# Kernel tuning notes

Hardware: AMD Instinct MI355X
Metric: run time of the kernel (lower is better)

The kernel has to match this reference:

```python
import jax, jax.numpy as jnp
import numpy as np

B, N1, N2, E = 8, 32, 32, 256
H = 8                 # num_heads == args.vir_heads
KD = E // H           # key dim per head = 32
HD = E // H           # head dim (value_dim == embed_dim)
L = N1 * N2           # 1024 tokens
SCALING = KD ** -0.5
LN_EPS = 1e-5


def _rel_pos_2d():
    # RetNetRelPosDeform2D with zero offsets (vir_use_deformable=False)
    half = 1.0 / 10000.0 ** jnp.linspace(0.0, 1.0, KD // 2)
    angle = jnp.repeat(half, 2)                                   # (KD,) interleaved pairs
    decay = jnp.log(1.0 - 2.0 ** (-2.0 - 5.0 * jnp.arange(H, dtype=jnp.float32) / H))  # (H,)
    i1 = jnp.arange(N1, dtype=jnp.float32)
    i2 = jnp.arange(N2, dtype=jnp.float32)
    index_k = (i1[:, None] + i2[None, :]).reshape(L)              # (L,)
    sin_k = jnp.sin(index_k[:, None] * angle[None, :])            # (L, KD)
    cos_k = jnp.cos(index_k[:, None] * angle[None, :])
    # zero offsets => index_q == index_k, broadcast over (B, H)
    sin_q = sin_k[None, None]                                     # (1,1,L,KD)
    cos_q = cos_k[None, None]
    # Manhattan distance decay mask on the 2D grid
    d = (jnp.abs(i1[:, None, None, None] - i1[None, None, :, None])
         + jnp.abs(i2[None, :, None, None] - i2[None, None, None, :])).reshape(L, L)
    mask = jnp.exp(d[None, :, :] * decay[:, None, None])          # (H, L, L)
    mask = jnp.nan_to_num(mask)
    mask = mask / jnp.sqrt(mask.sum(-1, keepdims=True))
    return sin_q, cos_q, sin_k, cos_k, mask


def rotate_every_two(x):
    x1 = x[..., ::2]
    x2 = x[..., 1::2]
    return jnp.stack((-x2, x1), axis=-1).reshape(x.shape)


def theta_shift(x, sin, cos):
    return x * cos + rotate_every_two(x) * sin


def setup_inputs() -> dict:
    key = jax.random.key(0)
    ks = jax.random.split(key, 5)
    gain_qkv = 2.0 ** -2.5 * (6.0 / (E + E)) ** 0.5  # xavier_uniform bound scale
    gain_o = 2.0 ** -1 * (6.0 / (E + E)) ** 0.5
    x = jax.random.normal(ks[0], (B, N1, N2, E), dtype=jnp.float32)
    Wq = jax.random.uniform(ks[1], (E, E), jnp.float32, -gain_qkv, gain_qkv)
    Wk = jax.random.uniform(ks[2], (E, E), jnp.float32, -gain_qkv, gain_qkv)
    Wv = jax.random.uniform(ks[3], (E, E), jnp.float32, -gain_qkv, gain_qkv)
    Wo = jax.random.uniform(ks[4], (E, E), jnp.float32, -gain_o, gain_o)
    ln_g = jnp.ones((HD,), jnp.float32)
    ln_b = jnp.zeros((HD,), jnp.float32)
    return {"x": x, "Wq": Wq, "Wk": Wk, "Wv": Wv, "Wo": Wo, "ln_g": ln_g, "ln_b": ln_b}


def reference(x, Wq, Wk, Wv, Wo, ln_g, ln_b):
    sin_q, cos_q, sin_k, cos_k, mask = _rel_pos_2d()
    xf = x.reshape(B, L, E)
    q = (xf @ Wq.T).reshape(B, L, H, KD).transpose(0, 2, 1, 3)    # (B,H,L,KD)
    k = (xf @ Wk.T * SCALING).reshape(B, L, H, KD).transpose(0, 2, 1, 3)
    vr = (xf @ Wv.T).reshape(B, L, H, HD).transpose(0, 2, 1, 3)   # (B,H,L,HD)
    qr = theta_shift(q, sin_q, cos_q)
    kr = theta_shift(k, sin_k[None, None], cos_k[None, None])
    qk = jnp.einsum('bhqd,bhkd->bhqk', qr, kr) * mask[None]       # (B,H,L,L)
    den = jnp.clip(jax.lax.stop_gradient(jnp.abs(qk)).sum(-1, keepdims=True), 1.0, 5e4)
    qk = qk / den
    out = jnp.einsum('bhqk,bhkd->bhqd', qk, vr).transpose(0, 2, 1, 3)  # (B,L,H,HD)
    mu = out.mean(-1, keepdims=True)
    var = out.var(-1, keepdims=True)
    out = (out - mu) / jnp.sqrt(var + LN_EPS) * ln_g + ln_b       # per-head LayerNorm
    out = jax.nn.gelu(out.reshape(B, L, H * HD), approximate=False)
    out = out @ Wo.T
    return out.reshape(B, N1, N2, E)
```

## Files before the change

kernel.cpp:

```cpp
#include <hip/hip_runtime.h>
#include <math.h>

typedef unsigned short u16;
typedef unsigned int u32;
typedef __bf16 bf16x8 __attribute__((ext_vector_type(8)));
typedef float f32x4 __attribute__((ext_vector_type(4)));

#define SCALING 0.17677669529663687f
#define LOG2E 1.44269504088896f
#define LOG2_10000 13.287712379549449f

__device__ __forceinline__ u16 f2bf(float f) {
    u32 u; __builtin_memcpy(&u, &f, 4);
    u = u + 0x7FFFu + ((u >> 16) & 1u);
    return (u16)(u >> 16);
}
__device__ __forceinline__ u32 fbits(float f) {
    u32 u; __builtin_memcpy(&u, &f, 4); return u;
}
__device__ __forceinline__ u32 pack_bf16(float lo, float hi) {
    return __builtin_amdgcn_perm(fbits(hi) + 0x8000u, fbits(lo) + 0x8000u, 0x07060302u);
}
__device__ __forceinline__ f32x4 mfma16(bf16x8 a, bf16x8 b, f32x4 c) {
    return __builtin_amdgcn_mfma_f32_16x16x32_bf16(a, b, c, 0, 0, 0);
}
__device__ __forceinline__ float decay_l2(int h) {
    return logf(1.0f - exp2f(-2.0f - 0.625f * (float)h)) * LOG2E;
}

__global__ __launch_bounds__(256) void cvt_kernel(
    const float* __restrict__ x,
    const float* __restrict__ Wq, const float* __restrict__ Wk,
    const float* __restrict__ Wv, const float* __restrict__ Wo,
    u16* __restrict__ xb, u16* __restrict__ wb) {
    int bid = blockIdx.x;
    const float* src; u16* dst; int off;
    if (bid < 1024) { src = x; dst = xb; off = bid * 2048; }
    else {
        int wsel = (bid - 1024) >> 5;
        src = (wsel == 0) ? Wq : (wsel == 1) ? Wk : (wsel == 2) ? Wv : Wo;
        dst = wb + wsel * 65536;
        off = ((bid - 1024) & 31) * 2048;
    }
    int i = off + threadIdx.x * 8;
    float4 a = *(const float4*)&src[i];
    float4 b = *(const float4*)&src[i + 4];
    union { int4 v; u16 s[8]; } t;
    t.s[0] = f2bf(a.x); t.s[1] = f2bf(a.y); t.s[2] = f2bf(a.z); t.s[3] = f2bf(a.w);
    t.s[4] = f2bf(b.x); t.s[5] = f2bf(b.y); t.s[6] = f2bf(b.z); t.s[7] = f2bf(b.w);
    *(int4*)&dst[i] = t.v;
}

__global__ __launch_bounds__(256) void gemm_bt_kernel(
    const u16* __restrict__ A, const u16* __restrict__ Wb,
    u16* __restrict__ O0, u16* __restrict__ O1, u16* __restrict__ O2,
    float* __restrict__ Of, int mode_base) {
    __shared__ __align__(16) u16 As[64 * 136];
    __shared__ __align__(16) u16 Ws[64 * 136];
    int z = blockIdx.z;
    const u16* W = Wb + z * 65536;
    u16* O = (z == 0) ? O0 : (z == 1) ? O1 : O2;
    int mode = mode_base + z;
    int n0 = blockIdx.x * 64, r0 = blockIdx.y * 64;
    int tid = threadIdx.x;
    int w = tid >> 6, lane = tid & 63, ln = lane & 15, quad = lane >> 4;
    f32x4 acc[4] = {};
#pragma unroll
    for (int ch = 0; ch < 2; ch++) {
        int k0 = ch * 128;
        if (ch) __syncthreads();
#pragma unroll
        for (int i = 0; i < 4; i++) {
            int c = tid + i * 256;
            int row = c >> 4, seg = c & 15;
            *(int4*)&As[row * 136 + seg * 8] = *(const int4*)&A[(long)(r0 + row) * 256 + k0 + seg * 8];
            *(int4*)&Ws[row * 136 + seg * 8] = *(const int4*)&W[(long)(n0 + row) * 256 + k0 + seg * 8];
        }
        __syncthreads();
#pragma unroll
        for (int kt = 0; kt < 4; kt++) {
            bf16x8 a = *(const bf16x8*)&As[(w * 16 + ln) * 136 + kt * 32 + quad * 8];
#pragma unroll
            for (int nt = 0; nt < 4; nt++) {
                bf16x8 b = *(const bf16x8*)&Ws[(nt * 16 + ln) * 136 + kt * 32 + quad * 8];
                acc[nt] = mfma16(a, b, acc[nt]);
            }
        }
    }
    int rowg = r0 + w * 16 + quad * 4;
    if (mode == 3) {
#pragma unroll
        for (int nt = 0; nt < 4; nt++) {
            int e = n0 + nt * 16 + ln;
#pragma unroll
            for (int r = 0; r < 4; r++)
                Of[(long)(rowg + r) * 256 + e] = acc[nt][r];
        }
        return;
    }
    float scl = (mode == 1) ? SCALING : 1.0f;
#pragma unroll
    for (int nt = 0; nt < 4; nt++) {
        int e = n0 + nt * 16 + ln;
        int d = e & 31, hh = e >> 5;
        float ang = exp2f(-LOG2_10000 * (1.0f / 15.0f) * (float)(d >> 1));
#pragma unroll
        for (int r = 0; r < 4; r++) {
            int gi = rowg + r;
            int b = gi >> 10, l = gi & 1023;
            float v = acc[nt][r] * scl;
            float p = __shfl_xor(v, 1);
            float res;
            if (mode == 2) {
                res = v;
            } else {
                float idx = (float)((l >> 5) + (l & 31));
                float sv, cv;
                __sincosf(idx * ang, &sv, &cv);
                res = (d & 1) ? (v * cv + p * sv) : (v * cv - p * sv);
            }
            O[(((long)(b * 8 + hh)) * 1024 + l) * 32 + d] = f2bf(res);
        }
    }
}

__global__ __launch_bounds__(256) void attn_kernel(
    const u16* __restrict__ qr, const u16* __restrict__ kr, const u16* __restrict__ vr,
    const float* __restrict__ lng, const float* __restrict__ lnb,
    u16* __restrict__ out) {
    __shared__ __align__(16) u16 Qs[64 * 40];
    __shared__ __align__(16) u16 Ks[2][64 * 40];
    __shared__ __align__(16) u32 VtW[2][32 * 36];
    __shared__ __align__(16) u32 PsW[4][16 * 36];
    __shared__ float Tt[64];
    __shared__ float Ss[32];
    __shared__ float lngS[32], lnbS[32];
    int b = blockIdx.z, h = blockIdx.y, q0 = blockIdx.x * 64;
    int tid = threadIdx.x, w = tid >> 6, lane = tid & 63, ln = lane & 15, quad = lane >> 4;
    long bh = b * 8 + h;
    const u16* qb = qr + bh * 32768;
    const u16* kb = kr + bh * 32768;
    const u16* vb = vr + bh * 32768;
    float dec = decay_l2(h);
    {
        int row = tid >> 2, seg = tid & 3;
        *(int4*)&Qs[row * 40 + seg * 8] = *(const int4*)&qb[(q0 + row) * 32 + seg * 8];
    }
    if (tid < 63) Tt[tid] = exp2f(dec * (float)tid);
    if (tid >= 64 && tid < 96) { lngS[tid - 64] = lng[tid - 64]; lnbS[tid - 64] = lnb[tid - 64]; }
    int krow = tid >> 2, kseg = tid & 3;
    int vp = tid >> 3, vseg = tid & 7;
    int4 kreg = *(const int4*)&kb[(long)krow * 32 + kseg * 8];
    int2 v0 = *(const int2*)&vb[(long)(vp * 2) * 32 + vseg * 4];
    int2 v1 = *(const int2*)&vb[(long)(vp * 2 + 1) * 32 + vseg * 4];
    __syncthreads();
    if (tid < 32) {
        float s = 0.0f;
#pragma unroll
        for (int b2 = 0; b2 < 32; b2++) s += Tt[abs(tid - b2)];
        Ss[tid] = s;
    }
    *(int4*)&Ks[0][krow * 40 + kseg * 8] = kreg;
    VtW[0][(vseg * 4 + 0) * 36 + vp] = __builtin_amdgcn_perm(v1.x, v0.x, 0x05040100u);
    VtW[0][(vseg * 4 + 1) * 36 + vp] = __builtin_amdgcn_perm(v1.x, v0.x, 0x07060302u);
    VtW[0][(vseg * 4 + 2) * 36 + vp] = __builtin_amdgcn_perm(v1.y, v0.y, 0x05040100u);
    VtW[0][(vseg * 4 + 3) * 36 + vp] = __builtin_amdgcn_perm(v1.y, v0.y, 0x07060302u);
    kreg = *(const int4*)&kb[(long)(64 + krow) * 32 + kseg * 8];
    v0 = *(const int2*)&vb[(long)(64 + vp * 2) * 32 + vseg * 4];
    v1 = *(const int2*)&vb[(long)(64 + vp * 2 + 1) * 32 + vseg * 4];
    __syncthreads();
    int q = q0 + w * 16 + ln;
    int q1i = q >> 5, q2i = q & 31;
    float rqv = rsqrtf(Ss[q1i] * Ss[q2i]);
    bf16x8 aq = *(const bf16x8*)&Qs[(w * 16 + ln) * 40 + quad * 8];
    float bt[2][4];
#pragma unroll
    for (int s2 = 0; s2 < 2; s2++)
#pragma unroll
        for (int r = 0; r < 4; r++)
            bt[s2][r] = Tt[abs(q2i - (s2 * 16 + quad * 4 + r))];
    f32x4 accO0 = {}, accO1 = {};
    float den = 0.0f;
    u32* psw = &PsW[w][0];
    for (int kt = 0; kt < 16; kt++) {
        int cur = kt & 1;
        float a0 = Tt[abs(q1i - 2 * kt)] * rqv;
        float a1 = Tt[abs(q1i - 2 * kt - 1)] * rqv;
        const u16* ksb = &Ks[cur][0];
        const u32* vtb = &VtW[cur][0];
#pragma unroll
        for (int nt = 0; nt < 4; nt++) {
            bf16x8 ak = *(const bf16x8*)&ksb[(nt * 16 + ln) * 40 + quad * 8];
            f32x4 s = mfma16(ak, aq, (f32x4){0.f, 0.f, 0.f, 0.f});
            float aa = (nt & 2) ? a1 : a0;
            float p0 = s[0] * aa * bt[nt & 1][0];
            float p1 = s[1] * aa * bt[nt & 1][1];
            float p2 = s[2] * aa * bt[nt & 1][2];
            float p3 = s[3] * aa * bt[nt & 1][3];
            den += fabsf(p0); den += fabsf(p1); den += fabsf(p2); den += fabsf(p3);
            int2 pw;
            pw.x = (int)pack_bf16(p0, p1);
            pw.y = (int)pack_bf16(p2, p3);
            *(int2*)&psw[ln * 36 + nt * 8 + quad * 2] = pw;
        }
#pragma unroll
        for (int c = 0; c < 2; c++) {
            bf16x8 bp  = *(const bf16x8*)&psw[ln * 36 + c * 16 + quad * 4];
            bf16x8 av0 = *(const bf16x8*)&vtb[(ln)      * 36 + c * 16 + quad * 4];
            bf16x8 av1 = *(const bf16x8*)&vtb[(16 + ln) * 36 + c * 16 + quad * 4];
            accO0 = mfma16(av0, bp, accO0);
            accO1 = mfma16(av1, bp, accO1);
        }
        if (kt < 15) {
            int nb = 1 - cur;
            *(int4*)&Ks[nb][krow * 40 + kseg * 8] = kreg;
            VtW[nb][(vseg * 4 + 0) * 36 + vp] = __builtin_amdgcn_perm(v1.x, v0.x, 0x05040100u);
            VtW[nb][(vseg * 4 + 1) * 36 + vp] = __builtin_amdgcn_perm(v1.x, v0.x, 0x07060302u);
            VtW[nb][(vseg * 4 + 2) * 36 + vp] = __builtin_amdgcn_perm(v1.y, v0.y, 0x05040100u);
            VtW[nb][(vseg * 4 + 3) * 36 + vp] = __builtin_amdgcn_perm(v1.y, v0.y, 0x07060302u);
            if (kt < 14) {
                int t2 = (kt + 2) * 64;
                kreg = *(const int4*)&kb[(long)(t2 + krow) * 32 + kseg * 8];
                v0 = *(const int2*)&vb[(long)(t2 + vp * 2) * 32 + vseg * 4];
                v1 = *(const int2*)&vb[(long)(t2 + vp * 2 + 1) * 32 + vseg * 4];
            }
            __syncthreads();
        }
    }
    den += __shfl_xor(den, 16);
    den += __shfl_xor(den, 32);
    float id = 1.0f / fminf(fmaxf(den, 1.0f), 50000.0f);
    float o[8];
#pragma unroll
    for (int r = 0; r < 4; r++) { o[r] = accO0[r] * id; o[4 + r] = accO1[r] * id; }
    float s1 = 0.0f, s2 = 0.0f;
#pragma unroll
    for (int i = 0; i < 8; i++) { s1 += o[i]; s2 += o[i] * o[i]; }
    s1 += __shfl_xor(s1, 16); s1 += __shfl_xor(s1, 32);
    s2 += __shfl_xor(s2, 16); s2 += __shfl_xor(s2, 32);
    float mean = s1 * (1.0f / 32.0f);
    float var = s2 * (1.0f / 32.0f) - mean * mean;
    float rstd = rsqrtf(var + 1e-5f);
    float xg[8];
#pragma unroll
    for (int nv = 0; nv < 2; nv++)
#pragma unroll
        for (int r = 0; r < 4; r++) {
            int d = nv * 16 + quad * 4 + r;
            float xv = (o[nv * 4 + r] - mean) * rstd * lngS[d] + lnbS[d];
            xg[nv * 4 + r] = 0.5f * xv * (1.0f + erff(xv * 0.70710678118654752f));
        }
    u16* orow = out + ((long)(b * 1024 + q)) * 256 + h * 32;
    int2 st0, st1;
    st0.x = (int)pack_bf16(xg[0], xg[1]); st0.y = (int)pack_bf16(xg[2], xg[3]);
    st1.x = (int)pack_bf16(xg[4], xg[5]); st1.y = (int)pack_bf16(xg[6], xg[7]);
    *(int2*)&orow[quad * 4] = st0;
    *(int2*)&orow[16 + quad * 4] = st1;
}

extern "C" void kernel_launch(void* const* d_in, const int* in_sizes, int n_in,
                              void* d_out, int out_size, void* d_ws, size_t ws_size,
                              hipStream_t stream) {
    const float* x   = (const float*)d_in[0];
    const float* Wq  = (const float*)d_in[1];
    const float* Wk  = (const float*)d_in[2];
    const float* Wv  = (const float*)d_in[3];
    const float* Wo  = (const float*)d_in[4];
    const float* lng = (const float*)d_in[5];
    const float* lnb = (const float*)d_in[6];
    float* outp = (float*)d_out;

    u16* xb   = (u16*)d_ws;
    u16* wb   = xb + 2097152;
    u16* qr   = wb + 262144;
    u16* kr   = qr + 2097152;
    u16* vr   = kr + 2097152;
    u16* attn = vr + 2097152;

    cvt_kernel<<<1152, 256, 0, stream>>>(x, Wq, Wk, Wv, Wo, xb, wb);
    gemm_bt_kernel<<<dim3(4, 128, 3), 256, 0, stream>>>(xb, wb, qr, kr, vr, nullptr, 0);
    attn_kernel<<<dim3(16, 8, 8), 256, 0, stream>>>(qr, kr, vr, lng, lnb, attn);
    gemm_bt_kernel<<<dim3(4, 128, 1), 256, 0, stream>>>(attn, wb + 3 * 65536, nullptr, nullptr, nullptr, outp, 3);
}
```

Measured before the change: 114.8 us.

## Fuse fp32-to-bf16 conversion into GEMM loads and keep P in registers

Removes the separate conversion kernel: the QKV projection now reads fp32 x and fp32 weights directly and converts to bf16 while staging into shared memory, and the output projection converts Wo on the fly. Rotary sin/cos values move into a small precomputed table kernel that the GEMM epilogue reads. In attention, the probability tile no longer goes through shared memory; it is packed in registers and fed to a 16x16x16 bf16 MFMA whose B-operand layout matches the QK output. The layernorm parameters are read from global memory instead of shared, which cuts a conversion pass and LDS traffic. In exchange the GEMM repeats weight conversion in every block and issues more, smaller MFMAs.

```diff
diff --git a/kernel.cpp b/kernel.cpp
--- a/kernel.cpp
+++ b/kernel.cpp
@@ -3,7 +3,9 @@
 
 typedef unsigned short u16;
 typedef unsigned int u32;
+typedef unsigned long long u64;
 typedef __bf16 bf16x8 __attribute__((ext_vector_type(8)));
+typedef short s16x4 __attribute__((ext_vector_type(4)));
 typedef float f32x4 __attribute__((ext_vector_type(4)));
 
 #define SCALING 0.17677669529663687f
@@ -24,41 +26,48 @@
 __device__ __forceinline__ f32x4 mfma16(bf16x8 a, bf16x8 b, f32x4 c) {
     return __builtin_amdgcn_mfma_f32_16x16x32_bf16(a, b, c, 0, 0, 0);
 }
+__device__ __forceinline__ f32x4 mfma_k16(u64 a, u64 b, f32x4 c) {
+#if __has_builtin(__builtin_amdgcn_mfma_f32_16x16x16bf16_1k)
+    s16x4 av, bv;
+    __builtin_memcpy(&av, &a, 8); __builtin_memcpy(&bv, &b, 8);
+    return __builtin_amdgcn_mfma_f32_16x16x16bf16_1k(av, bv, c, 0, 0, 0);
+#elif __has_builtin(__builtin_amdgcn_mfma_f32_16x16x16_bf16)
+    typedef __bf16 bf16x4_t __attribute__((ext_vector_type(4)));
+    bf16x4_t av, bv;
+    __builtin_memcpy(&av, &a, 8); __builtin_memcpy(&bv, &b, 8);
+    return __builtin_amdgcn_mfma_f32_16x16x16_bf16(av, bv, c, 0, 0, 0);
+#else
+    f32x4 d = c;
+    asm volatile("v_mfma_f32_16x16x16_bf16 %0, %1, %2, %0\n\ts_nop 4"
+                 : "+v"(d) : "v"(a), "v"(b));
+    return d;
+#endif
+}
 __device__ __forceinline__ float decay_l2(int h) {
     return logf(1.0f - exp2f(-2.0f - 0.625f * (float)h)) * LOG2E;
 }
 
-__global__ __launch_bounds__(256) void cvt_kernel(
-    const float* __restrict__ x,
-    const float* __restrict__ Wq, const float* __restrict__ Wk,
-    const float* __restrict__ Wv, const float* __restrict__ Wo,
-    u16* __restrict__ xb, u16* __restrict__ wb) {
-    int bid = blockIdx.x;
-    const float* src; u16* dst; int off;
-    if (bid < 1024) { src = x; dst = xb; off = bid * 2048; }
-    else {
-        int wsel = (bid - 1024) >> 5;
-        src = (wsel == 0) ? Wq : (wsel == 1) ? Wk : (wsel == 2) ? Wv : Wo;
-        dst = wb + wsel * 65536;
-        off = ((bid - 1024) & 31) * 2048;
-    }
-    int i = off + threadIdx.x * 8;
-    float4 a = *(const float4*)&src[i];
-    float4 b = *(const float4*)&src[i + 4];
-    union { int4 v; u16 s[8]; } t;
-    t.s[0] = f2bf(a.x); t.s[1] = f2bf(a.y); t.s[2] = f2bf(a.z); t.s[3] = f2bf(a.w);
-    t.s[4] = f2bf(b.x); t.s[5] = f2bf(b.y); t.s[6] = f2bf(b.z); t.s[7] = f2bf(b.w);
-    *(int4*)&dst[i] = t.v;
-}
-
+__global__ __launch_bounds__(256) void tc_kernel(float2* __restrict__ tc) {
+    int idx = blockIdx.x * 256 + threadIdx.x;
+    int l = idx >> 5, d = idx & 31;
+    float ang = exp2f(-LOG2_10000 * (1.0f / 15.0f) * (float)(d >> 1));
+    float idl = (float)((l >> 5) + (l & 31));
+    float sv, cv;
+    __sincosf(idl * ang, &sv, &cv);
+    tc[idx] = make_float2(cv, (d & 1) ? sv : -sv);
+}
+
+template<int AF32>
 __global__ __launch_bounds__(256) void gemm_bt_kernel(
-    const u16* __restrict__ A, const u16* __restrict__ Wb,
+    const void* __restrict__ Av,
+    const float* __restrict__ W0, const float* __restrict__ W1, const float* __restrict__ W2,
+    const float2* __restrict__ tc,
     u16* __restrict__ O0, u16* __restrict__ O1, u16* __restrict__ O2,
     float* __restrict__ Of, int mode_base) {
     __shared__ __align__(16) u16 As[64 * 136];
     __shared__ __align__(16) u16 Ws[64 * 136];
     int z = blockIdx.z;
-    const u16* W = Wb + z * 65536;
+    const float* W = (z == 0) ? W0 : (z == 1) ? W1 : W2;
     u16* O = (z == 0) ? O0 : (z == 1) ? O1 : O2;
     int mode = mode_base + z;
     int n0 = blockIdx.x * 64, r0 = blockIdx.y * 64;
@@ -70,11 +79,33 @@
         int k0 = ch * 128;
         if (ch) __syncthreads();
 #pragma unroll
-        for (int i = 0; i < 4; i++) {
+        for (int i = 0; i < 8; i++) {
             int c = tid + i * 256;
-            int row = c >> 4, seg = c & 15;
-            *(int4*)&As[row * 136 + seg * 8] = *(const int4*)&A[(long)(r0 + row) * 256 + k0 + seg * 8];
-            *(int4*)&Ws[row * 136 + seg * 8] = *(const int4*)&W[(long)(n0 + row) * 256 + k0 + seg * 8];
+            int row = c >> 5, seg = c & 31;
+            float4 wv = *(const float4*)&W[(long)(n0 + row) * 256 + k0 + seg * 4];
+            union { int2 v; u16 s[4]; } t;
+            t.s[0] = f2bf(wv.x); t.s[1] = f2bf(wv.y); t.s[2] = f2bf(wv.z); t.s[3] = f2bf(wv.w);
+            *(int2*)&Ws[row * 136 + seg * 4] = t.v;
+        }
+        if (AF32) {
+            const float* A = (const float*)Av;
+#pragma unroll
+            for (int i = 0; i < 8; i++) {
+                int c = tid + i * 256;
+                int row = c >> 5, seg = c & 31;
+                float4 av = *(const float4*)&A[(long)(r0 + row) * 256 + k0 + seg * 4];
+                union { int2 v; u16 s[4]; } t;
+                t.s[0] = f2bf(av.x); t.s[1] = f2bf(av.y); t.s[2] = f2bf(av.z); t.s[3] = f2bf(av.w);
+                *(int2*)&As[row * 136 + seg * 4] = t.v;
+            }
+        } else {
+            const u16* A = (const u16*)Av;
+#pragma unroll
+            for (int i = 0; i < 4; i++) {
+                int c = tid + i * 256;
+                int row = c >> 4, seg = c & 15;
+                *(int4*)&As[row * 136 + seg * 8] = *(const int4*)&A[(long)(r0 + row) * 256 + k0 + seg * 8];
+            }
         }
         __syncthreads();
 #pragma unroll
@@ -103,7 +134,6 @@
     for (int nt = 0; nt < 4; nt++) {
         int e = n0 + nt * 16 + ln;
         int d = e & 31, hh = e >> 5;
-        float ang = exp2f(-LOG2_10000 * (1.0f / 15.0f) * (float)(d >> 1));
 #pragma unroll
         for (int r = 0; r < 4; r++) {
             int gi = rowg + r;
@@ -114,10 +144,8 @@
             if (mode == 2) {
                 res = v;
             } else {
-                float idx = (float)((l >> 5) + (l & 31));
-                float sv, cv;
-                __sincosf(idx * ang, &sv, &cv);
-                res = (d & 1) ? (v * cv + p * sv) : (v * cv - p * sv);
+                float2 sc = tc[l * 32 + d];
+                res = v * sc.x + p * sc.y;
             }
             O[(((long)(b * 8 + hh)) * 1024 + l) * 32 + d] = f2bf(res);
         }
@@ -131,10 +159,8 @@
     __shared__ __align__(16) u16 Qs[64 * 40];
     __shared__ __align__(16) u16 Ks[2][64 * 40];
     __shared__ __align__(16) u32 VtW[2][32 * 36];
-    __shared__ __align__(16) u32 PsW[4][16 * 36];
     __shared__ float Tt[64];
     __shared__ float Ss[32];
-    __shared__ float lngS[32], lnbS[32];
     int b = blockIdx.z, h = blockIdx.y, q0 = blockIdx.x * 64;
     int tid = threadIdx.x, w = tid >> 6, lane = tid & 63, ln = lane & 15, quad = lane >> 4;
     long bh = b * 8 + h;
@@ -147,13 +173,21 @@
         *(int4*)&Qs[row * 40 + seg * 8] = *(const int4*)&qb[(q0 + row) * 32 + seg * 8];
     }
     if (tid < 63) Tt[tid] = exp2f(dec * (float)tid);
-    if (tid >= 64 && tid < 96) { lngS[tid - 64] = lng[tid - 64]; lnbS[tid - 64] = lnb[tid - 64]; }
     int krow = tid >> 2, kseg = tid & 3;
     int vp = tid >> 3, vseg = tid & 7;
     int4 kreg = *(const int4*)&kb[(long)krow * 32 + kseg * 8];
     int2 v0 = *(const int2*)&vb[(long)(vp * 2) * 32 + vseg * 4];
     int2 v1 = *(const int2*)&vb[(long)(vp * 2 + 1) * 32 + vseg * 4];
     __syncthreads();
+    bf16x8 aq = *(const bf16x8*)&Qs[(w * 16 + ln) * 40 + quad * 8];
+    int q = q0 + w * 16 + ln;
+    int q1i = q >> 5, q2i = q & 31;
+    float bt[2][4];
+#pragma unroll
+    for (int s2 = 0; s2 < 2; s2++)
+#pragma unroll
+        for (int r = 0; r < 4; r++)
+            bt[s2][r] = Tt[abs(q2i - (s2 * 16 + quad * 4 + r))];
     if (tid < 32) {
         float s = 0.0f;
 #pragma unroll
@@ -169,19 +203,9 @@
     v0 = *(const int2*)&vb[(long)(64 + vp * 2) * 32 + vseg * 4];
     v1 = *(const int2*)&vb[(long)(64 + vp * 2 + 1) * 32 + vseg * 4];
     __syncthreads();
-    int q = q0 + w * 16 + ln;
-    int q1i = q >> 5, q2i = q & 31;
     float rqv = rsqrtf(Ss[q1i] * Ss[q2i]);
-    bf16x8 aq = *(const bf16x8*)&Qs[(w * 16 + ln) * 40 + quad * 8];
-    float bt[2][4];
-#pragma unroll
-    for (int s2 = 0; s2 < 2; s2++)
-#pragma unroll
-        for (int r = 0; r < 4; r++)
-            bt[s2][r] = Tt[abs(q2i - (s2 * 16 + quad * 4 + r))];
     f32x4 accO0 = {}, accO1 = {};
     float den = 0.0f;
-    u32* psw = &PsW[w][0];
     for (int kt = 0; kt < 16; kt++) {
         int cur = kt & 1;
         float a0 = Tt[abs(q1i - 2 * kt)] * rqv;
@@ -198,18 +222,12 @@
             float p2 = s[2] * aa * bt[nt & 1][2];
             float p3 = s[3] * aa * bt[nt & 1][3];
             den += fabsf(p0); den += fabsf(p1); den += fabsf(p2); den += fabsf(p3);
-            int2 pw;
-            pw.x = (int)pack_bf16(p0, p1);
-            pw.y = (int)pack_bf16(p2, p3);
-            *(int2*)&psw[ln * 36 + nt * 8 + quad * 2] = pw;
-        }
-#pragma unroll
-        for (int c = 0; c < 2; c++) {
-            bf16x8 bp  = *(const bf16x8*)&psw[ln * 36 + c * 16 + quad * 4];
-            bf16x8 av0 = *(const bf16x8*)&vtb[(ln)      * 36 + c * 16 + quad * 4];
-            bf16x8 av1 = *(const bf16x8*)&vtb[(16 + ln) * 36 + c * 16 + quad * 4];
-            accO0 = mfma16(av0, bp, accO0);
-            accO1 = mfma16(av1, bp, accO1);
+            u32 blo = pack_bf16(p0, p1), bhi = pack_bf16(p2, p3);
+            u64 bb = ((u64)bhi << 32) | blo;
+            u64 av0 = *(const u64*)&vtb[ln * 36 + nt * 8 + quad * 2];
+            u64 av1 = *(const u64*)&vtb[(16 + ln) * 36 + nt * 8 + quad * 2];
+            accO0 = mfma_k16(av0, bb, accO0);
+            accO1 = mfma_k16(av1, bb, accO1);
         }
         if (kt < 15) {
             int nb = 1 - cur;
@@ -247,7 +265,7 @@
 #pragma unroll
         for (int r = 0; r < 4; r++) {
             int d = nv * 16 + quad * 4 + r;
-            float xv = (o[nv * 4 + r] - mean) * rstd * lngS[d] + lnbS[d];
+            float xv = (o[nv * 4 + r] - mean) * rstd * lng[d] + lnb[d];
             xg[nv * 4 + r] = 0.5f * xv * (1.0f + erff(xv * 0.70710678118654752f));
         }
     u16* orow = out + ((long)(b * 1024 + q)) * 256 + h * 32;
@@ -270,15 +288,14 @@
     const float* lnb = (const float*)d_in[6];
     float* outp = (float*)d_out;
 
-    u16* xb   = (u16*)d_ws;
-    u16* wb   = xb + 2097152;
-    u16* qr   = wb + 262144;
-    u16* kr   = qr + 2097152;
-    u16* vr   = kr + 2097152;
-    u16* attn = vr + 2097152;
-
-    cvt_kernel<<<1152, 256, 0, stream>>>(x, Wq, Wk, Wv, Wo, xb, wb);
-    gemm_bt_kernel<<<dim3(4, 128, 3), 256, 0, stream>>>(xb, wb, qr, kr, vr, nullptr, 0);
-    attn_kernel<<<dim3(16, 8, 8), 256, 0, stream>>>(qr, kr, vr, lng, lnb, attn);
-    gemm_bt_kernel<<<dim3(4, 128, 1), 256, 0, stream>>>(attn, wb + 3 * 65536, nullptr, nullptr, nullptr, outp, 3);
-}
+    u16* qr    = (u16*)d_ws;
+    u16* kr    = qr + 2097152;
+    u16* vr    = kr + 2097152;
+    u16* attnb = vr + 2097152;
+    float2* tc = (float2*)(attnb + 2097152);
+
+    tc_kernel<<<128, 256, 0, stream>>>(tc);
+    gemm_bt_kernel<1><<<dim3(4, 128, 3), 256, 0, stream>>>(x, Wq, Wk, Wv, tc, qr, kr, vr, nullptr, 0);
+    attn_kernel<<<dim3(16, 8, 8), 256, 0, stream>>>(qr, kr, vr, lng, lnb, attnb);
+    gemm_bt_kernel<0><<<dim3(4, 128, 1), 256, 0, stream>>>(attnb, Wo, Wo, Wo, tc, nullptr, nullptr, nullptr, outp, 3);
+}
```

Result: slower. 120.5 us (+4.9%).
